# Performance work log

Measured on AMD Instinct MI355X. Metric: run time of the kernel, lower is better.

The kernel has to match this reference:

```python
import jax, jax.numpy as jnp
import numpy as np

B = 8        # batch
L = 512      # context length (time steps) == seq_len
DV = 512     # number of variables (token/sequence dim for Mamba)
DM = 512     # d_model
PL = 96      # pred_len
EL = 3       # e_layers
DS = 16      # d_state
DC = 4       # d_conv
EXP = 2
DI = EXP * DM          # d_inner = 1024
DTR = (DM + 15) // 16  # dt_rank = 32
NM = 2 * EL            # Mamba instances: fwd+bwd per layer


def setup_inputs():
    key = jax.random.key(0)
    ks = jax.random.split(key, 16)
    def g(i, shape, s=0.02):
        return jax.random.normal(ks[i], shape, dtype=jnp.float32) * s
    A_log = jnp.tile(jnp.log(jnp.arange(1, DS + 1, dtype=jnp.float32))[None, None, :], (NM, DI, 1))
    return {
        "x": jax.random.normal(ks[0], (B, L, DV), dtype=jnp.float32),
        "emb_w": g(1, (DM, L)), "emb_b": jnp.zeros((DM,), jnp.float32),
        "ln_g": jnp.ones((EL, DM), jnp.float32), "ln_b": jnp.zeros((EL, DM), jnp.float32),
        "m_in_w": g(2, (NM, 2 * DI, DM)),
        "m_conv_w": g(3, (NM, DI, DC), 0.1),
        "m_conv_b": jnp.zeros((NM, DI), jnp.float32),
        "m_xp_w": g(4, (NM, DTR + 2 * DS, DI)),
        "m_dt_w": g(5, (NM, DI, DTR), 0.1),
        "m_dt_b": g(6, (NM, DI), 0.5),
        "m_A_log": A_log,
        "m_D": jnp.ones((NM, DI), jnp.float32),
        "m_out_w": g(7, (NM, DM, DI)),
        "ffn_ln_g": jnp.ones((EL, DM), jnp.float32), "ffn_ln_b": jnp.zeros((EL, DM), jnp.float32),
        "ffn_w1": g(8, (EL, 4 * DM, DM)), "ffn_b1": jnp.zeros((EL, 4 * DM), jnp.float32),
        "ffn_w2": g(9, (EL, DM, 4 * DM)), "ffn_b2": jnp.zeros((EL, DM), jnp.float32),
        "enc_g": jnp.ones((DM,), jnp.float32), "enc_b": jnp.zeros((DM,), jnp.float32),
        "proj_w": g(10, (PL, DM)), "proj_b": jnp.zeros((PL,), jnp.float32),
    }


def layer_norm(x, g, b):
    mu = x.mean(-1, keepdims=True)
    v = ((x - mu) ** 2).mean(-1, keepdims=True)
    return (x - mu) * jax.lax.rsqrt(v + 1e-5) * g + b


def mamba(x, in_w, conv_w, conv_b, xp_w, dt_w, dt_b, A_log, Dp, out_w):
    # x: [B, S, DM]; selective-scan Mamba block (mamba_ssm reference math)
    Bb, S, _ = x.shape
    xz = jnp.einsum('bsd,ed->bse', x, in_w)          # [B,S,2*DI]
    xc, z = jnp.split(xz, 2, axis=-1)
    # causal depthwise conv1d (padding=DC-1, truncate to S)
    xpad = jnp.pad(xc, ((0, 0), (DC - 1, 0), (0, 0)))
    xc = sum(xpad[:, k:k + S, :] * conv_w[:, k] for k in range(DC)) + conv_b
    xc = jax.nn.silu(xc)
    xdbl = jnp.einsum('bsi,ei->bse', xc, xp_w)       # [B,S,DTR+2*DS]
    dt_lo = xdbl[..., :DTR]
    Bm = xdbl[..., DTR:DTR + DS]
    Cm = xdbl[..., DTR + DS:]
    dt = jax.nn.softplus(jnp.einsum('bsr,ir->bsi', dt_lo, dt_w) + dt_b)  # [B,S,DI]
    A = -jnp.exp(A_log)                               # [DI,DS]

    def step(h, t):
        dt_t, B_t, C_t, u_t = t                       # [B,DI],[B,DS],[B,DS],[B,DI]
        dA = jnp.exp(dt_t[..., None] * A)             # [B,DI,DS]
        h = dA * h + (dt_t * u_t)[..., None] * B_t[:, None, :]
        y = jnp.einsum('bis,bs->bi', h, C_t)
        return h, y

    xs = (dt.swapaxes(0, 1), Bm.swapaxes(0, 1), Cm.swapaxes(0, 1), xc.swapaxes(0, 1))
    h0 = jnp.zeros((Bb, DI, DS), dtype=x.dtype)
    _, ys = jax.lax.scan(step, h0, xs)
    y = ys.swapaxes(0, 1) + xc * Dp
    y = y * jax.nn.silu(z)
    return jnp.einsum('bsi,di->bsd', y, out_w)


def reference(x, emb_w, emb_b, ln_g, ln_b, m_in_w, m_conv_w, m_conv_b, m_xp_w,
              m_dt_w, m_dt_b, m_A_log, m_D, m_out_w, ffn_ln_g, ffn_ln_b,
              ffn_w1, ffn_b1, ffn_w2, ffn_b2, enc_g, enc_b, proj_w, proj_b):
    # per-sample instance norm over time (means detached, as in torch)
    means = jax.lax.stop_gradient(x.mean(axis=1, keepdims=True))   # [B,1,DV]
    xc = x - means
    stdev = jnp.sqrt((xc ** 2).mean(axis=1, keepdims=True) + 1e-5)  # [B,1,DV]
    x_norm = xc / stdev
    # inverted time embedding: [B,L,DV] -> [B,DV,DM]
    h = jnp.einsum('bld,ml->bdm', x_norm, emb_w) + emb_b
    for i in range(EL):
        hn = layer_norm(h, ln_g[i], ln_b[i])
        yf = mamba(hn, m_in_w[2 * i], m_conv_w[2 * i], m_conv_b[2 * i], m_xp_w[2 * i],
                   m_dt_w[2 * i], m_dt_b[2 * i], m_A_log[2 * i], m_D[2 * i], m_out_w[2 * i])
        yb = mamba(hn[:, ::-1, :], m_in_w[2 * i + 1], m_conv_w[2 * i + 1], m_conv_b[2 * i + 1],
                   m_xp_w[2 * i + 1], m_dt_w[2 * i + 1], m_dt_b[2 * i + 1], m_A_log[2 * i + 1],
                   m_D[2 * i + 1], m_out_w[2 * i + 1])[:, ::-1, :]
        h = h + (yf + yb) / 2.0
        f = layer_norm(h, ffn_ln_g[i], ffn_ln_b[i])
        f = jax.nn.gelu(jnp.einsum('bdm,hm->bdh', f, ffn_w1[i]) + ffn_b1[i], approximate=False)
        h = h + jnp.einsum('bdh,mh->bdm', f, ffn_w2[i]) + ffn_b2[i]
    h = layer_norm(h, enc_g, enc_b)
    y = jnp.einsum('bdm,pm->bdp', h, proj_w) + proj_b   # [B,DV,PL]
    y = y.swapaxes(1, 2)                                 # [B,PL,DV]
    y = y + x_norm[:, -1:, :]                            # last-step residual baseline
    y = y * stdev + means                                # de-normalize
    return y


if __name__ == '__main__':
    out = reference(**setup_inputs())
    print(out.shape)
```

## Files before the change

kernel.cpp:

```cpp
#include <hip/hip_runtime.h>
#include <hip/hip_bf16.h>
#include <math.h>

#define B_ 8
#define L_ 512
#define DV_ 512
#define DM_ 512
#define PL_ 96
#define EL_ 3
#define DS_ 16
#define DC_ 4
#define DI_ 1024
#define DTR_ 32
#define S_ 512
#define M_ 4096
#define CH_ 16
#define CS_ 32

typedef float f32x4 __attribute__((ext_vector_type(4)));
typedef short bf16x8 __attribute__((ext_vector_type(8)));
typedef short bf16x4 __attribute__((ext_vector_type(4)));

__device__ __forceinline__ float bf2f(short s) {
  unsigned u = ((unsigned)(unsigned short)s) << 16;
  return __builtin_bit_cast(float, u);
}
__device__ __forceinline__ short f2bf(float f) {
  unsigned u = __builtin_bit_cast(unsigned, f);
  u = u + 0x7FFFu + ((u >> 16) & 1u);
  return (short)(u >> 16);
}
__device__ __forceinline__ float h2f(unsigned short u) {
  _Float16 h = __builtin_bit_cast(_Float16, u);
  return (float)h;
}
__device__ __forceinline__ unsigned short f2h(float f) {
  _Float16 h = (_Float16)f;
  return __builtin_bit_cast(unsigned short, h);
}

__device__ __forceinline__ void gload16(const short* g, short* l) {
  __builtin_amdgcn_global_load_lds(
      (const __attribute__((address_space(1))) void*)g,
      (__attribute__((address_space(3))) void*)l, 16, 0, 0);
}

#define WC0 65536
#define WC1 (WC0 + 1572864)
#define WC2 (WC1 + 98304)
#define WC3 (WC2 + 49152)
#define WC4 (WC3 + 786432)
#define WC5 (WC4 + 786432)
#define WC6 (WC5 + 786432)
#define WC7 (WC6 + 12288)

__global__ __launch_bounds__(256)
void wcvt_k(const float* __restrict__ e, const float* __restrict__ iw,
            const float* __restrict__ xp, const float* __restrict__ dtw,
            const float* __restrict__ ow, const float* __restrict__ w1,
            const float* __restrict__ w2, const float* __restrict__ pw,
            short* __restrict__ de, short* __restrict__ di,
            short* __restrict__ dxp, short* __restrict__ ddt,
            short* __restrict__ dow, short* __restrict__ dw1,
            short* __restrict__ dw2, short* __restrict__ dpw)
{
  int idx = blockIdx.x * 256 + threadIdx.x;
  const float* s; short* d; int off;
  if (idx < WC0)      { s = e;   d = de;  off = idx; }
  else if (idx < WC1) { s = iw;  d = di;  off = idx - WC0; }
  else if (idx < WC2) { s = xp;  d = dxp; off = idx - WC1; }
  else if (idx < WC3) { s = dtw; d = ddt; off = idx - WC2; }
  else if (idx < WC4) { s = ow;  d = dow; off = idx - WC3; }
  else if (idx < WC5) { s = w1;  d = dw1; off = idx - WC4; }
  else if (idx < WC6) { s = w2;  d = dw2; off = idx - WC5; }
  else                { s = pw;  d = dpw; off = idx - WC6; }
  float4 v = ((const float4*)s)[off];
  union { short sh[4]; int2 p; } r;
  r.sh[0] = f2bf(v.x); r.sh[1] = f2bf(v.y);
  r.sh[2] = f2bf(v.z); r.sh[3] = f2bf(v.w);
  ((int2*)d)[off] = r.p;
}

__global__ __launch_bounds__(256)
void stats_k(const float* __restrict__ x, float* __restrict__ means,
             float* __restrict__ stdev, float* __restrict__ rstd,
             float* __restrict__ xlast)
{
  int d = blockIdx.x * 256 + threadIdx.x;
  int b = blockIdx.y;
  const float* xp = x + (size_t)b * L_ * DV_ + d;
  float s = 0.f, ss = 0.f;
  for (int l = 0; l < L_; l++) {
    float v = xp[(size_t)l * DV_];
    s += v; ss += v * v;
  }
  float mu = s / (float)L_;
  float var = ss / (float)L_ - mu * mu;
  float sd = sqrtf(var + 1e-5f);
  float rs = 1.f / sd;
  int idx = b * DV_ + d;
  means[idx] = mu; stdev[idx] = sd; rstd[idx] = rs;
  xlast[idx] = (xp[(size_t)(L_ - 1) * DV_] - mu) * rs;
}

__global__ __launch_bounds__(256)
void tnorm_k(const float* __restrict__ x, const float* __restrict__ means,
             const float* __restrict__ rstd, short* __restrict__ xnT)
{
  __shared__ float tile[64][65];
  const int t = threadIdx.x;
  const int j = t & 63;
  const int i0 = t >> 6;
  const int bz = blockIdx.z;
  const int l0 = blockIdx.y << 6;
  const int d0 = blockIdx.x << 6;
  const float* xp = x + ((size_t)bz * L_ + l0) * DV_ + d0;
  #pragma unroll
  for (int i = i0; i < 64; i += 4) tile[i][j] = xp[(size_t)i * DV_ + j];
  __syncthreads();
  short* op = xnT + ((size_t)bz * DV_ + d0) * L_ + l0;
  const int sb = bz * DV_ + d0;
  #pragma unroll
  for (int i = i0; i < 64; i += 4) {
    float mu = means[sb + i];
    float rs = rstd[sb + i];
    op[(size_t)i * L_ + j] = f2bf((tile[j][i] - mu) * rs);
  }
}

template <int ADD>
__global__ __launch_bounds__(256)
void ln_k(float* __restrict__ X, const short* __restrict__ add,
          const float* __restrict__ abias,
          const float* __restrict__ g, const float* __restrict__ b,
          short* __restrict__ Y)
{
  int row = blockIdx.x;
  float* x = X + (size_t)row * DM_;
  int t = threadIdx.x;
  float v0 = x[t], v1 = x[t + 256];
  if constexpr (ADD >= 1) {
    v0 += bf2f(add[(size_t)row * DM_ + t]);
    v1 += bf2f(add[(size_t)row * DM_ + t + 256]);
    if constexpr (ADD == 2) { v0 += abias[t]; v1 += abias[t + 256]; }
    x[t] = v0; x[t + 256] = v1;
  }
  float s = v0 + v1, ss = v0 * v0 + v1 * v1;
  #pragma unroll
  for (int o = 1; o < 64; o <<= 1) { s += __shfl_xor(s, o); ss += __shfl_xor(ss, o); }
  __shared__ float sb[8];
  int wave = t >> 6, lane = t & 63;
  if (lane == 0) { sb[wave] = s; sb[4 + wave] = ss; }
  __syncthreads();
  s = sb[0] + sb[1] + sb[2] + sb[3];
  ss = sb[4] + sb[5] + sb[6] + sb[7];
  float mu = s / (float)DM_;
  float var = ss / (float)DM_ - mu * mu;
  float rs = rsqrtf(var + 1e-5f);
  Y[(size_t)row * DM_ + t]       = f2bf((v0 - mu) * rs * g[t]       + b[t]);
  Y[(size_t)row * DM_ + t + 256] = f2bf((v1 - mu) * rs * g[t + 256] + b[t + 256]);
}

template <int REV>
__global__ __launch_bounds__(256)
void conv_k(const short* __restrict__ xcin, const float* __restrict__ w,
            const float* __restrict__ cb, short* __restrict__ xcout)
{
  int idx = blockIdx.x * 256 + threadIdx.x;
  int ig = (idx & 127) << 3;
  int bs = idx >> 7;
  int tt0 = bs & (S_ - 1);
  int b = bs >> 9;
  const short* u = xcin + (size_t)(b * S_) * DI_ + ig;
  float4 wv[8];
  #pragma unroll
  for (int n = 0; n < 8; n++) wv[n] = *(const float4*)(w + (ig + n) * DC_);
  float acc[8];
  {
    float4 c0 = *(const float4*)(cb + ig);
    float4 c1 = *(const float4*)(cb + ig + 4);
    acc[0] = c0.x; acc[1] = c0.y; acc[2] = c0.z; acc[3] = c0.w;
    acc[4] = c1.x; acc[5] = c1.y; acc[6] = c1.z; acc[7] = c1.w;
  }
  #pragma unroll
  for (int k = 0; k < DC_; k++) {
    int tt = REV ? (tt0 + (DC_ - 1) - k) : (tt0 - (DC_ - 1) + k);
    if (tt >= 0 && tt < S_) {
      bf16x8 uv = *(const bf16x8*)(u + (size_t)tt * DI_);
      #pragma unroll
      for (int n = 0; n < 8; n++) {
        float wk = (k == 0) ? wv[n].x : (k == 1) ? wv[n].y
                 : (k == 2) ? wv[n].z : wv[n].w;
        acc[n] += wk * bf2f(uv[n]);
      }
    }
  }
  union { short sh[8]; bf16x8 v; } r;
  #pragma unroll
  for (int n = 0; n < 8; n++) {
    float sig = 1.f / (1.f + __expf(-acc[n]));
    r.sh[n] = f2bf(acc[n] * sig);
  }
  *(bf16x8*)(xcout + ((size_t)bs << 10) + ig) = r.v;
}

__global__ __launch_bounds__(256)
void scan_p1(const unsigned short* __restrict__ dt16, const short* __restrict__ xc,
             const short* __restrict__ xdbl, const float* __restrict__ A_log,
             unsigned short* __restrict__ part_h, unsigned short* __restrict__ part_A)
{
  const int gid = blockIdx.x * 256 + threadIdx.x;
  const int q = gid & 3;
  const int i = (gid >> 2) & (DI_ - 1);
  const int b = (gid >> 12) & (B_ - 1);
  const int dir = gid >> 15;
  const int c = blockIdx.y;
  float Ai[4];
  const float* al = A_log + (size_t)dir * DI_ * DS_ + i * DS_ + q * 4;
  #pragma unroll
  for (int n = 0; n < 4; n++) Ai[n] = -__expf(al[n]);

  const int ti0 = dir ? (S_ - 1 - c * CS_) : (c * CS_);
  const size_t dof = (size_t)dir * M_ * DI_;
  const unsigned short* pdt = dt16 + dof + ((size_t)b * S_ + ti0) * DI_ + i;
  const short* pu = xc + dof + ((size_t)b * S_ + ti0) * DI_ + i;
  const short* pbc = xdbl + (size_t)dir * M_ * 64 +
                     (((size_t)b * S_ + ti0) << 6) + DTR_ + q * 4;
  const int sstep = dir ? -DI_ : DI_;
  const int sbc = dir ? -64 : 64;

  float h[4];
  #pragma unroll
  for (int n = 0; n < 4; n++) h[n] = 0.f;
  float dsum = 0.f;

  #pragma unroll 4
  for (int sl = 0; sl < CS_; sl++) {
    float dtv = h2f(*pdt);
    float u = bf2f(*pu);
    bf16x4 vB = *(const bf16x4*)pbc;
    float du = dtv * u;
    dsum += dtv;
    #pragma unroll
    for (int n = 0; n < 4; n++) {
      float dA = __expf(dtv * Ai[n]);
      h[n] = dA * h[n] + du * bf2f(vB[n]);
    }
    pdt += sstep; pu += sstep; pbc += sbc;
  }
  union { unsigned short s[4]; int2 v; } uh, ua;
  #pragma unroll
  for (int n = 0; n < 4; n++) {
    uh.s[n] = f2h(h[n]);
    ua.s[n] = f2h(__expf(Ai[n] * dsum));
  }
  const size_t ix = ((((size_t)c * 2 * B_ + dir * B_ + b) * DI_ + i) << 4) + (q << 2);
  *(int2*)(part_h + ix) = uh.v;
  *(int2*)(part_A + ix) = ua.v;
}

__global__ __launch_bounds__(256)
void scan_p2(unsigned short* __restrict__ part_h,
             const unsigned short* __restrict__ part_A)
{
  const size_t gid = (size_t)blockIdx.x * 256 + threadIdx.x;
  const size_t stride = (size_t)2 * B_ * DI_ * DS_;
  float hin = 0.f;
  #pragma unroll
  for (int c = 0; c < CH_; c++) {
    size_t ix = (size_t)c * stride + gid;
    float hh = h2f(part_h[ix]);
    float pA = h2f(part_A[ix]);
    part_h[ix] = f2h(hin);
    hin = hh + pA * hin;
  }
}

__global__ __launch_bounds__(256)
void scan_p3(unsigned short* dt16, const short* __restrict__ xc,
             const short* __restrict__ xdbl, const short* __restrict__ zb,
             const float* __restrict__ A_log, const float* __restrict__ Dp,
             const unsigned short* __restrict__ part_h)
{
  const int gid = blockIdx.x * 256 + threadIdx.x;
  const int q = gid & 3;
  const int i = (gid >> 2) & (DI_ - 1);
  const int b = (gid >> 12) & (B_ - 1);
  const int dir = gid >> 15;
  const int c = blockIdx.y;
  float Ai[4];
  const float* al = A_log + (size_t)dir * DI_ * DS_ + i * DS_ + q * 4;
  #pragma unroll
  for (int n = 0; n < 4; n++) Ai[n] = -__expf(al[n]);
  const float Di = Dp[(size_t)dir * DI_ + i];

  float h[4];
  {
    const size_t ix = ((((size_t)c * 2 * B_ + dir * B_ + b) * DI_ + i) << 4) + (q << 2);
    union { unsigned short s[4]; int2 v; } uh;
    uh.v = *(const int2*)(part_h + ix);
    #pragma unroll
    for (int n = 0; n < 4; n++) h[n] = h2f(uh.s[n]);
  }

  const int ti0 = dir ? (S_ - 1 - c * CS_) : (c * CS_);
  const size_t dof = (size_t)dir * M_ * DI_;
  unsigned short* pdt = dt16 + dof + ((size_t)b * S_ + ti0) * DI_ + i;
  const short* pu = xc + dof + ((size_t)b * S_ + ti0) * DI_ + i;
  const short* pbc = xdbl + (size_t)dir * M_ * 64 +
                     (((size_t)b * S_ + ti0) << 6) + DTR_ + q * 4;
  const short* pz = zb + dof + ((size_t)b * S_ + ti0) * DI_ + i;
  const int sstep = dir ? -DI_ : DI_;
  const int sbc = dir ? -64 : 64;

  #pragma unroll 4
  for (int sl = 0; sl < CS_; sl++) {
    float dtv = h2f(*pdt);
    float u = bf2f(*pu);
    bf16x4 vB = *(const bf16x4*)pbc;
    bf16x4 vC = *(const bf16x4*)(pbc + DS_);
    float zv = bf2f(*pz);
    float du = dtv * u;
    float yp = 0.f;
    #pragma unroll
    for (int n = 0; n < 4; n++) {
      float dA = __expf(dtv * Ai[n]);
      h[n] = dA * h[n] + du * bf2f(vB[n]);
      yp += h[n] * bf2f(vC[n]);
    }
    yp += __shfl_xor(yp, 1);
    yp += __shfl_xor(yp, 2);
    float sil = zv / (1.f + __expf(-zv));
    float yv = (yp + u * Di) * sil;
    if (q == 0) *(short*)pdt = f2bf(yv);
    pdt += sstep; pu += sstep; pbc += sbc; pz += sstep;
  }
}

enum { EPI_F32_BIAS, EPI_BF16, EPI_F16_SOFTPLUS, EPI_HALF_BF16, EPI_GELU,
       EPI_PROJ, EPI_INPROJ };

template <int EPI, int BM, int BN, int BK>
__global__ __launch_bounds__(256)
void gemm_k(const short* __restrict__ A0, const short* __restrict__ A1,
            const short* __restrict__ W0, const short* __restrict__ W1,
            int khalf, int mhalf, int N, int K, int lda, int ldw,
            float* __restrict__ Cf, short* __restrict__ Cb, int ldc,
            const float* __restrict__ bias,
            const float* __restrict__ xlast, const float* __restrict__ stdev,
            const float* __restrict__ means)
{
  constexpr int MT = BM / 32;
  constexpr int NT = BN / 32;
  constexpr int KS = BK / 32;
  constexpr int CHK = BK / 8;
  constexpr int MSK = CHK - 1;
  constexpr int NA = (BM * CHK) / 256;
  constexpr int NW = (BN * CHK) / 256;
  constexpr int VC = NA + NW;
  __shared__ __align__(16) short As[3][BM * BK];
  __shared__ __align__(16) short Ws[3][BN * BK];
  const int tid = threadIdx.x;
  const int m0 = blockIdx.x * BM;
  const int n0 = blockIdx.y * BN;
  const int wave = tid >> 6, lane = tid & 63;
  const int wm = (wave & 1) * (BM / 2), wn = (wave >> 1) * (BN / 2);
  const int quad = lane >> 4, l16 = lane & 15;

  const short* W0m = (m0 < mhalf) ? W0 : W1;

  f32x4 acc[MT][NT] = {};

  size_t aoff[NA];
  #pragma unroll
  for (int j = 0; j < NA; j++) {
    int id = j * 256 + tid;
    int r = id / CHK, qp = id % CHK;
    aoff[j] = (size_t)(m0 + r) * lda + ((qp ^ (r & MSK)) << 3);
  }
  size_t woff[NW];
  #pragma unroll
  for (int j = 0; j < NW; j++) {
    int id = j * 256 + tid;
    int r = id / CHK, qp = id % CHK;
    int wr = n0 + r; if (wr > N - 1) wr = N - 1;
    woff[j] = (size_t)wr * ldw + ((qp ^ (r & MSK)) << 3);
  }
  const int lbase = wave * 512;

  const int KB = K / BK;

  auto stage = [&](int slab, int bi) {
    const int k0 = slab * BK;
    const short* Ab = (k0 < khalf) ? A0 + k0 : A1 + (k0 - khalf);
    const short* Wb = (k0 < khalf) ? W0m + k0 : W1 + (k0 - khalf);
    #pragma unroll
    for (int j = 0; j < NA; j++)
      gload16(Ab + aoff[j], &As[bi][j * 2048 + lbase]);
    #pragma unroll
    for (int j = 0; j < NW; j++)
      gload16(Wb + woff[j], &Ws[bi][j * 2048 + lbase]);
  };

  stage(0, 0);
  if (KB > 1) stage(1, 1);
  __builtin_amdgcn_sched_barrier(0);
  if (KB > 1) asm volatile("s_waitcnt vmcnt(%0)" :: "n"(VC) : "memory");
  else        asm volatile("s_waitcnt vmcnt(0)" ::: "memory");
  __builtin_amdgcn_s_barrier();
  __builtin_amdgcn_sched_barrier(0);

  int cur = 0, nxt = 2;
  for (int kb = 0; kb < KB; kb++) {
    if (kb + 2 < KB) {
      stage(kb + 2, nxt);
      __builtin_amdgcn_sched_barrier(0);
    }
    bf16x8 af[MT][KS], bfr[NT][KS];
    #pragma unroll
    for (int mt = 0; mt < MT; mt++)
      #pragma unroll
      for (int st = 0; st < KS; st++)
        af[mt][st] = *(const bf16x8*)(&As[cur][0] + (wm + mt * 16 + l16) * BK +
                                      (((st * 4 + quad) ^ (l16 & MSK)) << 3));
    #pragma unroll
    for (int nt = 0; nt < NT; nt++)
      #pragma unroll
      for (int st = 0; st < KS; st++)
        bfr[nt][st] = *(const bf16x8*)(&Ws[cur][0] + (wn + nt * 16 + l16) * BK +
                                       (((st * 4 + quad) ^ (l16 & MSK)) << 3));
    #pragma unroll
    for (int st = 0; st < KS; st++)
      #pragma unroll
      for (int mt = 0; mt < MT; mt++)
        #pragma unroll
        for (int nt = 0; nt < NT; nt++)
          acc[mt][nt] = __builtin_amdgcn_mfma_f32_16x16x32_bf16(
              af[mt][st], bfr[nt][st], acc[mt][nt], 0, 0, 0);
    if (kb + 1 < KB) {
      __builtin_amdgcn_sched_barrier(0);
      if (kb + 2 < KB) asm volatile("s_waitcnt vmcnt(%0)" :: "n"(VC) : "memory");
      else             asm volatile("s_waitcnt vmcnt(0)" ::: "memory");
      __builtin_amdgcn_s_barrier();
      __builtin_amdgcn_sched_barrier(0);
      cur = (cur == 2) ? 0 : cur + 1;
      nxt = (nxt == 2) ? 0 : nxt + 1;
    }
  }

  const int boff = (m0 < mhalf) ? 0 : N;

  #pragma unroll
  for (int mt = 0; mt < MT; mt++) {
    #pragma unroll
    for (int nt = 0; nt < NT; nt++) {
      int n = n0 + wn + nt * 16 + l16;
      if (n >= N) continue;
      #pragma unroll
      for (int r = 0; r < 4; r++) {
        int m = m0 + wm + mt * 16 + quad * 4 + r;
        float v = acc[mt][nt][r];
        if constexpr (EPI == EPI_F32_BIAS) {
          Cf[(size_t)m * ldc + n] = v + bias[n];
        } else if constexpr (EPI == EPI_BF16) {
          Cb[(size_t)m * ldc + n] = f2bf(v);
        } else if constexpr (EPI == EPI_F16_SOFTPLUS) {
          float tt = v + bias[n + boff];
          float sp = (tt > 20.f) ? tt : log1pf(__expf(tt));
          ((unsigned short*)Cb)[(size_t)m * ldc + n] = f2h(sp);
        } else if constexpr (EPI == EPI_HALF_BF16) {
          Cb[(size_t)m * ldc + n] = f2bf(0.5f * v);
        } else if constexpr (EPI == EPI_GELU) {
          float tt = v + bias[n];
          Cb[(size_t)m * ldc + n] = f2bf(0.5f * tt * (1.f + erff(tt * 0.70710678118f)));
        } else if constexpr (EPI == EPI_PROJ) {
          int bb = m >> 9, d = m & 511;
          float tt = v + bias[n] + xlast[m];
          tt = tt * stdev[m] + means[m];
          Cf[((size_t)bb * PL_ + n) * DV_ + d] = tt;
        } else if constexpr (EPI == EPI_INPROJ) {
          if (n < DI_) Cb[(size_t)m * ldc + n] = f2bf(v);
          else ((short*)Cf)[(size_t)m * DI_ + (n - DI_)] = f2bf(v);
        }
      }
    }
  }
}

extern "C" void kernel_launch(void* const* d_in, const int* in_sizes, int n_in,
                              void* d_out, int out_size, void* d_ws, size_t ws_size,
                              hipStream_t stream)
{
  (void)in_sizes; (void)n_in; (void)out_size; (void)ws_size;
  const float* x        = (const float*)d_in[0];
  const float* emb_w    = (const float*)d_in[1];
  const float* emb_b    = (const float*)d_in[2];
  const float* ln_g     = (const float*)d_in[3];
  const float* ln_b     = (const float*)d_in[4];
  const float* m_in_w   = (const float*)d_in[5];
  const float* m_conv_w = (const float*)d_in[6];
  const float* m_conv_b = (const float*)d_in[7];
  const float* m_xp_w   = (const float*)d_in[8];
  const float* m_dt_w   = (const float*)d_in[9];
  const float* m_dt_b   = (const float*)d_in[10];
  const float* m_A_log  = (const float*)d_in[11];
  const float* m_D      = (const float*)d_in[12];
  const float* m_out_w  = (const float*)d_in[13];
  const float* ffn_ln_g = (const float*)d_in[14];
  const float* ffn_ln_b = (const float*)d_in[15];
  const float* ffn_w1   = (const float*)d_in[16];
  const float* ffn_b1   = (const float*)d_in[17];
  const float* ffn_w2   = (const float*)d_in[18];
  const float* ffn_b2   = (const float*)d_in[19];
  const float* enc_g    = (const float*)d_in[20];
  const float* enc_b    = (const float*)d_in[21];
  const float* proj_w   = (const float*)d_in[22];
  const float* proj_b   = (const float*)d_in[23];
  float* out = (float*)d_out;

  char* ws = (char*)d_ws;
  const size_t MB = 1024 * 1024;
  float* h      = (float*)(ws + 0);
  short* hn     = (short*)(ws + 8 * MB);
  short* ftmp   = (short*)(ws + 12 * MB);
  short* vtmp   = ftmp;
  short* scratch= (short*)(ws + 16 * MB);
  short* zbuf   = (short*)(ws + 24 * MB);
  short* xnT    = zbuf;
  short* f1out  = zbuf;
  short* xc     = (short*)(ws + 40 * MB);
  unsigned short* dtb = (unsigned short*)(ws + 56 * MB);
  short* xdbl   = (short*)(ws + 72 * MB);
  float* stats  = (float*)(ws + 73 * MB);
  unsigned short* part_A = (unsigned short*)(ws + 8 * MB);
  unsigned short* part_h = (unsigned short*)(ws + 16 * MB);
  float* means = stats, *stdevp = stats + 4096, *rstd = stats + 8192, *xlast = stats + 12288;

  short* emb_wb = (short*)(ws + 80 * MB);
  short* in_wb  = emb_wb + 262144;
  short* xp_wb  = in_wb  + 6291456;
  short* dt_wb  = xp_wb  + 393216;
  short* out_wb = dt_wb  + 196608;
  short* w1b    = out_wb + 3145728;
  short* w2b    = w1b    + 3145728;
  short* projb  = w2b    + 3145728;

  dim3 blk(256);
  const int NOSPLIT = 1 << 30;

  wcvt_k<<<dim3(16240), blk, 0, stream>>>(
      emb_w, m_in_w, m_xp_w, m_dt_w, m_out_w, ffn_w1, ffn_w2, proj_w,
      emb_wb, in_wb, xp_wb, dt_wb, out_wb, w1b, w2b, projb);

  stats_k<<<dim3(2, B_), blk, 0, stream>>>(x, means, stdevp, rstd, xlast);
  tnorm_k<<<dim3(8, 8, B_), blk, 0, stream>>>(x, means, rstd, xnT);
  gemm_k<EPI_F32_BIAS, 64, 32, 64><<<dim3(64, 16), blk, 0, stream>>>(
      xnT, xnT, emb_wb, emb_wb, NOSPLIT, NOSPLIT, DM_, L_, L_, L_,
      h, nullptr, DM_, emb_b, nullptr, nullptr, nullptr);

  for (int il = 0; il < EL_; il++) {
    if (il == 0)
      ln_k<0><<<dim3(4096), blk, 0, stream>>>(h, nullptr, nullptr, ln_g, ln_b, hn);
    else
      ln_k<2><<<dim3(4096), blk, 0, stream>>>(h, ftmp, ffn_b2 + (il - 1) * DM_,
          ln_g + il * DM_, ln_b + il * DM_, hn);
    for (int dir = 0; dir < 2; dir++) {
      int mod = 2 * il + dir;
      gemm_k<EPI_INPROJ, 64, 128, 32><<<dim3(64, 16), blk, 0, stream>>>(
          hn, hn, in_wb + (size_t)mod * 2 * DI_ * DM_,
          in_wb + (size_t)mod * 2 * DI_ * DM_, NOSPLIT, NOSPLIT,
          2 * DI_, DM_, DM_, DM_,
          (float*)(zbuf + (size_t)dir * M_ * DI_), scratch, DI_,
          nullptr, nullptr, nullptr, nullptr);
      if (dir == 0)
        conv_k<0><<<dim3(2048), blk, 0, stream>>>(
            scratch, m_conv_w + (size_t)mod * DI_ * DC_,
            m_conv_b + (size_t)mod * DI_, xc + (size_t)dir * M_ * DI_);
      else
        conv_k<1><<<dim3(2048), blk, 0, stream>>>(
            scratch, m_conv_w + (size_t)mod * DI_ * DC_,
            m_conv_b + (size_t)mod * DI_, xc + (size_t)dir * M_ * DI_);
    }
    gemm_k<EPI_BF16, 32, 32, 64><<<dim3(256, 2), blk, 0, stream>>>(
        xc, xc, xp_wb + (size_t)(2 * il) * 64 * DI_,
        xp_wb + (size_t)(2 * il + 1) * 64 * DI_, NOSPLIT, M_,
        64, DI_, DI_, DI_,
        nullptr, xdbl, 64, nullptr, nullptr, nullptr, nullptr);
    gemm_k<EPI_F16_SOFTPLUS, 64, 64, 32><<<dim3(128, 16), blk, 0, stream>>>(
        xdbl, xdbl, dt_wb + (size_t)(2 * il) * DI_ * DTR_,
        dt_wb + (size_t)(2 * il + 1) * DI_ * DTR_, NOSPLIT, M_,
        DI_, DTR_, 64, DTR_,
        nullptr, (short*)dtb, DI_, m_dt_b + (size_t)(2 * il) * DI_,
        nullptr, nullptr, nullptr);
    const float* Alog = m_A_log + (size_t)(2 * il) * DI_ * DS_;
    const float* Dp = m_D + (size_t)(2 * il) * DI_;
    scan_p1<<<dim3(256, CH_), blk, 0, stream>>>(dtb, xc, xdbl, Alog, part_h, part_A);
    scan_p2<<<dim3(1024), blk, 0, stream>>>(part_h, part_A);
    scan_p3<<<dim3(256, CH_), blk, 0, stream>>>(dtb, xc, xdbl, zbuf, Alog, Dp, part_h);
    gemm_k<EPI_HALF_BF16, 64, 32, 64><<<dim3(64, 16), blk, 0, stream>>>(
        (const short*)dtb, (const short*)(dtb + (size_t)M_ * DI_),
        out_wb + (size_t)(2 * il) * DM_ * DI_,
        out_wb + (size_t)(2 * il + 1) * DM_ * DI_,
        DI_, NOSPLIT, DM_, 2 * DI_, DI_, DI_,
        nullptr, vtmp, DM_, nullptr, nullptr, nullptr, nullptr);
    ln_k<1><<<dim3(4096), blk, 0, stream>>>(h, vtmp, nullptr,
        ffn_ln_g + il * DM_, ffn_ln_b + il * DM_, hn);
    gemm_k<EPI_GELU, 64, 128, 32><<<dim3(64, 16), blk, 0, stream>>>(
        hn, hn, w1b + (size_t)il * 4 * DM_ * DM_,
        w1b + (size_t)il * 4 * DM_ * DM_, NOSPLIT, NOSPLIT,
        4 * DM_, DM_, DM_, DM_,
        nullptr, f1out, 4 * DM_, ffn_b1 + (size_t)il * 4 * DM_,
        nullptr, nullptr, nullptr);
    gemm_k<EPI_BF16, 64, 32, 64><<<dim3(64, 16), blk, 0, stream>>>(
        f1out, f1out, w2b + (size_t)il * DM_ * 4 * DM_,
        w2b + (size_t)il * DM_ * 4 * DM_, NOSPLIT, NOSPLIT,
        DM_, 4 * DM_, 4 * DM_, 4 * DM_,
        nullptr, ftmp, DM_, nullptr, nullptr, nullptr, nullptr);
  }

  ln_k<2><<<dim3(4096), blk, 0, stream>>>(h, ftmp, ffn_b2 + 2 * DM_,
      enc_g, enc_b, hn);
  gemm_k<EPI_PROJ, 64, 32, 64><<<dim3(64, 3), blk, 0, stream>>>(
      hn, hn, projb, projb, NOSPLIT, NOSPLIT, PL_, DM_, DM_, DM_,
      out, nullptr, 0, proj_b, xlast, stdevp, means);
}
```

Baseline: 1.091 ms.

## Store backward-direction activations time-reversed so scans run forward with exp2

The in-projection GEMM for the backward direction now writes rows with the time index reversed within each sequence (m ^ (S-1)), so the conv and the scan kernels run a single forward-direction code path with no per-direction pointer strides. The out-projection GEMM reads the second half of its K dimension through reversed A-row offsets to undo the reversal. The scan kernels also fold log2(e) into A and use a hardware exp2, and process time steps in explicit groups of four. This removes direction branches and negative-stride addressing, and makes the exponentials cheaper. In exchange the GEMM loaders carry extra offset registers.

Result: no change. 1.080 ms (-1.0%).

```diff
diff --git a/kernel.cpp b/kernel.cpp
--- a/kernel.cpp
+++ b/kernel.cpp
@@ -16,6 +16,7 @@
 #define M_ 4096
 #define CH_ 16
 #define CS_ 32
+#define LOG2E_ 1.44269504088896f
 
 typedef float f32x4 __attribute__((ext_vector_type(4)));
 typedef short bf16x8 __attribute__((ext_vector_type(8)));
@@ -37,6 +38,14 @@
 __device__ __forceinline__ unsigned short f2h(float f) {
   _Float16 h = (_Float16)f;
   return __builtin_bit_cast(unsigned short, h);
+}
+
+__device__ __forceinline__ float exp2n(float x) {
+#if __has_builtin(__builtin_amdgcn_exp2f)
+  return __builtin_amdgcn_exp2f(x);
+#else
+  return __expf(x * 0.69314718055994531f);
+#endif
 }
 
 __device__ __forceinline__ void gload16(const short* g, short* l) {
@@ -161,7 +170,6 @@
   Y[(size_t)row * DM_ + t + 256] = f2bf((v1 - mu) * rs * g[t + 256] + b[t + 256]);
 }
 
-template <int REV>
 __global__ __launch_bounds__(256)
 void conv_k(const short* __restrict__ xcin, const float* __restrict__ w,
             const float* __restrict__ cb, short* __restrict__ xcout)
@@ -184,8 +192,8 @@
   }
   #pragma unroll
   for (int k = 0; k < DC_; k++) {
-    int tt = REV ? (tt0 + (DC_ - 1) - k) : (tt0 - (DC_ - 1) + k);
-    if (tt >= 0 && tt < S_) {
+    int tt = tt0 - (DC_ - 1) + k;
+    if (tt >= 0) {
       bf16x8 uv = *(const bf16x8*)(u + (size_t)tt * DI_);
       #pragma unroll
       for (int n = 0; n < 8; n++) {
@@ -215,44 +223,43 @@
   const int b = (gid >> 12) & (B_ - 1);
   const int dir = gid >> 15;
   const int c = blockIdx.y;
-  float Ai[4];
+  float Ai2[4];
   const float* al = A_log + (size_t)dir * DI_ * DS_ + i * DS_ + q * 4;
   #pragma unroll
-  for (int n = 0; n < 4; n++) Ai[n] = -__expf(al[n]);
-
-  const int ti0 = dir ? (S_ - 1 - c * CS_) : (c * CS_);
-  const size_t dof = (size_t)dir * M_ * DI_;
-  const unsigned short* pdt = dt16 + dof + ((size_t)b * S_ + ti0) * DI_ + i;
-  const short* pu = xc + dof + ((size_t)b * S_ + ti0) * DI_ + i;
+  for (int n = 0; n < 4; n++) Ai2[n] = -__expf(al[n]) * LOG2E_;
+
+  const size_t base = (size_t)dir * M_ * DI_ + ((size_t)b * S_ + c * CS_) * DI_ + i;
+  const unsigned short* pdt = dt16 + base;
+  const short* pu = xc + base;
   const short* pbc = xdbl + (size_t)dir * M_ * 64 +
-                     (((size_t)b * S_ + ti0) << 6) + DTR_ + q * 4;
-  const int sstep = dir ? -DI_ : DI_;
-  const int sbc = dir ? -64 : 64;
+                     (((size_t)b * S_ + c * CS_) << 6) + DTR_ + q * 4;
 
   float h[4];
   #pragma unroll
   for (int n = 0; n < 4; n++) h[n] = 0.f;
   float dsum = 0.f;
 
-  #pragma unroll 4
-  for (int sl = 0; sl < CS_; sl++) {
-    float dtv = h2f(*pdt);
-    float u = bf2f(*pu);
-    bf16x4 vB = *(const bf16x4*)pbc;
-    float du = dtv * u;
-    dsum += dtv;
-    #pragma unroll
-    for (int n = 0; n < 4; n++) {
-      float dA = __expf(dtv * Ai[n]);
-      h[n] = dA * h[n] + du * bf2f(vB[n]);
+  for (int s0 = 0; s0 < CS_; s0 += 4) {
+    #pragma unroll
+    for (int k = 0; k < 4; k++) {
+      float dtv = h2f(pdt[(size_t)k * DI_]);
+      float u = bf2f(pu[(size_t)k * DI_]);
+      bf16x4 vB = *(const bf16x4*)(pbc + k * 64);
+      float du = dtv * u;
+      dsum += dtv;
+      #pragma unroll
+      for (int n = 0; n < 4; n++) {
+        float dA = exp2n(dtv * Ai2[n]);
+        h[n] = dA * h[n] + du * bf2f(vB[n]);
+      }
     }
-    pdt += sstep; pu += sstep; pbc += sbc;
+    pdt += 4 * DI_; pu += 4 * DI_; pbc += 4 * 64;
   }
   union { unsigned short s[4]; int2 v; } uh, ua;
   #pragma unroll
   for (int n = 0; n < 4; n++) {
     uh.s[n] = f2h(h[n]);
-    ua.s[n] = f2h(__expf(Ai[n] * dsum));
+    ua.s[n] = f2h(exp2n(Ai2[n] * dsum));
   }
   const size_t ix = ((((size_t)c * 2 * B_ + dir * B_ + b) * DI_ + i) << 4) + (q << 2);
   *(int2*)(part_h + ix) = uh.v;
@@ -288,10 +295,10 @@
   const int b = (gid >> 12) & (B_ - 1);
   const int dir = gid >> 15;
   const int c = blockIdx.y;
-  float Ai[4];
+  float Ai2[4];
   const float* al = A_log + (size_t)dir * DI_ * DS_ + i * DS_ + q * 4;
   #pragma unroll
-  for (int n = 0; n < 4; n++) Ai[n] = -__expf(al[n]);
+  for (int n = 0; n < 4; n++) Ai2[n] = -__expf(al[n]) * LOG2E_;
   const float Di = Dp[(size_t)dir * DI_ + i];
 
   float h[4];
@@ -303,44 +310,43 @@
     for (int n = 0; n < 4; n++) h[n] = h2f(uh.s[n]);
   }
 
-  const int ti0 = dir ? (S_ - 1 - c * CS_) : (c * CS_);
-  const size_t dof = (size_t)dir * M_ * DI_;
-  unsigned short* pdt = dt16 + dof + ((size_t)b * S_ + ti0) * DI_ + i;
-  const short* pu = xc + dof + ((size_t)b * S_ + ti0) * DI_ + i;
+  const size_t base = (size_t)dir * M_ * DI_ + ((size_t)b * S_ + c * CS_) * DI_ + i;
+  unsigned short* pdt = dt16 + base;
+  const short* pu = xc + base;
+  const short* pz = zb + base;
   const short* pbc = xdbl + (size_t)dir * M_ * 64 +
-                     (((size_t)b * S_ + ti0) << 6) + DTR_ + q * 4;
-  const short* pz = zb + dof + ((size_t)b * S_ + ti0) * DI_ + i;
-  const int sstep = dir ? -DI_ : DI_;
-  const int sbc = dir ? -64 : 64;
-
-  #pragma unroll 4
-  for (int sl = 0; sl < CS_; sl++) {
-    float dtv = h2f(*pdt);
-    float u = bf2f(*pu);
-    bf16x4 vB = *(const bf16x4*)pbc;
-    bf16x4 vC = *(const bf16x4*)(pbc + DS_);
-    float zv = bf2f(*pz);
-    float du = dtv * u;
-    float yp = 0.f;
-    #pragma unroll
-    for (int n = 0; n < 4; n++) {
-      float dA = __expf(dtv * Ai[n]);
-      h[n] = dA * h[n] + du * bf2f(vB[n]);
-      yp += h[n] * bf2f(vC[n]);
+                     (((size_t)b * S_ + c * CS_) << 6) + DTR_ + q * 4;
+
+  for (int s0 = 0; s0 < CS_; s0 += 4) {
+    #pragma unroll
+    for (int k = 0; k < 4; k++) {
+      float dtv = h2f(pdt[(size_t)k * DI_]);
+      float u = bf2f(pu[(size_t)k * DI_]);
+      bf16x4 vB = *(const bf16x4*)(pbc + k * 64);
+      bf16x4 vC = *(const bf16x4*)(pbc + k * 64 + DS_);
+      float zv = bf2f(pz[(size_t)k * DI_]);
+      float du = dtv * u;
+      float yp = 0.f;
+      #pragma unroll
+      for (int n = 0; n < 4; n++) {
+        float dA = exp2n(dtv * Ai2[n]);
+        h[n] = dA * h[n] + du * bf2f(vB[n]);
+        yp += h[n] * bf2f(vC[n]);
+      }
+      yp += __shfl_xor(yp, 1);
+      yp += __shfl_xor(yp, 2);
+      float sil = zv / (1.f + __expf(-zv));
+      float yv = (yp + u * Di) * sil;
+      if (q == 0) *(short*)(pdt + (size_t)k * DI_) = f2bf(yv);
     }
-    yp += __shfl_xor(yp, 1);
-    yp += __shfl_xor(yp, 2);
-    float sil = zv / (1.f + __expf(-zv));
-    float yv = (yp + u * Di) * sil;
-    if (q == 0) *(short*)pdt = f2bf(yv);
-    pdt += sstep; pu += sstep; pbc += sbc; pz += sstep;
+    pdt += 4 * DI_; pu += 4 * DI_; pz += 4 * DI_; pbc += 4 * 64;
   }
 }
 
 enum { EPI_F32_BIAS, EPI_BF16, EPI_F16_SOFTPLUS, EPI_HALF_BF16, EPI_GELU,
-       EPI_PROJ, EPI_INPROJ };
-
-template <int EPI, int BM, int BN, int BK>
+       EPI_PROJ, EPI_INPROJ, EPI_INPROJ_REV };
+
+template <int EPI, int BM, int BN, int BK, int REVA = 0>
 __global__ __launch_bounds__(256)
 void gemm_k(const short* __restrict__ A0, const short* __restrict__ A1,
             const short* __restrict__ W0, const short* __restrict__ W1,
@@ -371,12 +377,14 @@
 
   f32x4 acc[MT][NT] = {};
 
-  size_t aoff[NA];
+  size_t aoff[NA], aoffR[REVA ? NA : 1];
   #pragma unroll
   for (int j = 0; j < NA; j++) {
     int id = j * 256 + tid;
     int r = id / CHK, qp = id % CHK;
     aoff[j] = (size_t)(m0 + r) * lda + ((qp ^ (r & MSK)) << 3);
+    if constexpr (REVA)
+      aoffR[j] = (size_t)((m0 + r) ^ (S_ - 1)) * lda + ((qp ^ (r & MSK)) << 3);
   }
   size_t woff[NW];
   #pragma unroll
@@ -394,9 +402,10 @@
     const int k0 = slab * BK;
     const short* Ab = (k0 < khalf) ? A0 + k0 : A1 + (k0 - khalf);
     const short* Wb = (k0 < khalf) ? W0m + k0 : W1 + (k0 - khalf);
+    const size_t* ao = (REVA && k0 >= khalf) ? aoffR : aoff;
     #pragma unroll
     for (int j = 0; j < NA; j++)
-      gload16(Ab + aoff[j], &As[bi][j * 2048 + lbase]);
+      gload16(Ab + ao[j], &As[bi][j * 2048 + lbase]);
     #pragma unroll
     for (int j = 0; j < NW; j++)
       gload16(Wb + woff[j], &Ws[bi][j * 2048 + lbase]);
@@ -481,6 +490,10 @@
         } else if constexpr (EPI == EPI_INPROJ) {
           if (n < DI_) Cb[(size_t)m * ldc + n] = f2bf(v);
           else ((short*)Cf)[(size_t)m * DI_ + (n - DI_)] = f2bf(v);
+        } else if constexpr (EPI == EPI_INPROJ_REV) {
+          int mr = m ^ (S_ - 1);
+          if (n < DI_) Cb[(size_t)mr * ldc + n] = f2bf(v);
+          else ((short*)Cf)[(size_t)mr * DI_ + (n - DI_)] = f2bf(v);
         }
       }
     }
@@ -566,20 +579,23 @@
           ln_g + il * DM_, ln_b + il * DM_, hn);
     for (int dir = 0; dir < 2; dir++) {
       int mod = 2 * il + dir;
-      gemm_k<EPI_INPROJ, 64, 128, 32><<<dim3(64, 16), blk, 0, stream>>>(
-          hn, hn, in_wb + (size_t)mod * 2 * DI_ * DM_,
-          in_wb + (size_t)mod * 2 * DI_ * DM_, NOSPLIT, NOSPLIT,
-          2 * DI_, DM_, DM_, DM_,
-          (float*)(zbuf + (size_t)dir * M_ * DI_), scratch, DI_,
-          nullptr, nullptr, nullptr, nullptr);
       if (dir == 0)
-        conv_k<0><<<dim3(2048), blk, 0, stream>>>(
-            scratch, m_conv_w + (size_t)mod * DI_ * DC_,
-            m_conv_b + (size_t)mod * DI_, xc + (size_t)dir * M_ * DI_);
+        gemm_k<EPI_INPROJ, 64, 128, 32><<<dim3(64, 16), blk, 0, stream>>>(
+            hn, hn, in_wb + (size_t)mod * 2 * DI_ * DM_,
+            in_wb + (size_t)mod * 2 * DI_ * DM_, NOSPLIT, NOSPLIT,
+            2 * DI_, DM_, DM_, DM_,
+            (float*)(zbuf + (size_t)dir * M_ * DI_), scratch, DI_,
+            nullptr, nullptr, nullptr, nullptr);
       else
-        conv_k<1><<<dim3(2048), blk, 0, stream>>>(
-            scratch, m_conv_w + (size_t)mod * DI_ * DC_,
-            m_conv_b + (size_t)mod * DI_, xc + (size_t)dir * M_ * DI_);
+        gemm_k<EPI_INPROJ_REV, 64, 128, 32><<<dim3(64, 16), blk, 0, stream>>>(
+            hn, hn, in_wb + (size_t)mod * 2 * DI_ * DM_,
+            in_wb + (size_t)mod * 2 * DI_ * DM_, NOSPLIT, NOSPLIT,
+            2 * DI_, DM_, DM_, DM_,
+            (float*)(zbuf + (size_t)dir * M_ * DI_), scratch, DI_,
+            nullptr, nullptr, nullptr, nullptr);
+      conv_k<<<dim3(2048), blk, 0, stream>>>(
+          scratch, m_conv_w + (size_t)mod * DI_ * DC_,
+          m_conv_b + (size_t)mod * DI_, xc + (size_t)dir * M_ * DI_);
     }
     gemm_k<EPI_BF16, 32, 32, 64><<<dim3(256, 2), blk, 0, stream>>>(
         xc, xc, xp_wb + (size_t)(2 * il) * 64 * DI_,
@@ -597,7 +613,7 @@
     scan_p1<<<dim3(256, CH_), blk, 0, stream>>>(dtb, xc, xdbl, Alog, part_h, part_A);
     scan_p2<<<dim3(1024), blk, 0, stream>>>(part_h, part_A);
     scan_p3<<<dim3(256, CH_), blk, 0, stream>>>(dtb, xc, xdbl, zbuf, Alog, Dp, part_h);
-    gemm_k<EPI_HALF_BF16, 64, 32, 64><<<dim3(64, 16), blk, 0, stream>>>(
+    gemm_k<EPI_HALF_BF16, 64, 32, 64, 1><<<dim3(64, 16), blk, 0, stream>>>(
         (const short*)dtb, (const short*)(dtb + (size_t)M_ * DI_),
         out_wb + (size_t)(2 * il) * DM_ * DI_,
         out_wb + (size_t)(2 * il + 1) * DM_ * DI_,
```
